# Kernel tuning notes

Measured on AMD Instinct MI355X. Metric: run time of the kernel, lower is better.

## Reference

```python
import jax, jax.numpy as jnp
import numpy as np

N_INST, L = 512, 512
VOCAB, EMB = 50000, 128
NF, K = 128, 3
HID = 3 * NF
ATT = 128
NCLS = 53


def setup_inputs() -> dict:
    key = jax.random.key(0)
    ks = jax.random.split(key, 10)
    char_ids = jax.random.randint(ks[0], (N_INST, L), 1, VOCAB)  # avoid pad_id=0
    pos_e1 = jax.random.randint(ks[1], (N_INST,), 0, L - 1)
    pos_e2 = jax.random.randint(ks[2], (N_INST,), 0, L - 1)
    emb = jax.random.normal(ks[3], (VOCAB, EMB), jnp.float32) * 0.02
    emb = emb.at[0].set(0.0)  # padding_idx = 0
    conv_w = jax.random.normal(ks[4], (NF, EMB, K), jnp.float32) * (1.0 / np.sqrt(EMB * K))
    conv_b = jnp.zeros((NF,), jnp.float32)
    W_w = jax.random.normal(ks[5], (ATT, HID), jnp.float32) * (1.0 / np.sqrt(HID))
    W_b = jnp.zeros((ATT,), jnp.float32)
    u_w = jax.random.normal(ks[6], (ATT,), jnp.float32) * (1.0 / np.sqrt(ATT))
    fc_w = jax.random.normal(ks[7], (NCLS, HID), jnp.float32) * (1.0 / np.sqrt(HID))
    fc_b = jnp.zeros((NCLS,), jnp.float32)
    return dict(char_ids=char_ids, pos_e1=pos_e1, pos_e2=pos_e2, emb=emb,
                conv_w=conv_w, conv_b=conv_b, W_w=W_w, W_b=W_b, u_w=u_w,
                fc_w=fc_w, fc_b=fc_b)


def _pcnn_pooled(char_ids, pos_e1, pos_e2, emb, conv_w, conv_b):
    # embedding lookup: (N, L, E) -> (N, E, L)
    x = jnp.transpose(emb[char_ids], (0, 2, 1))
    y = jax.lax.conv_general_dilated(
        x, conv_w, window_strides=(1,), padding=[(K // 2, K // 2)],
        dimension_numbers=('NCH', 'OIH', 'NCH'))
    y = jax.nn.relu(y + conv_b[None, :, None])  # (N, F, L)

    # per-row clamped/sorted boundaries (mirrors torch loop logic)
    e1 = jnp.minimum(pos_e1, pos_e2)
    e2 = jnp.maximum(pos_e1, pos_e2)
    e1 = jnp.clip(e1, 0, L)
    e2 = jnp.clip(e2, 0, L)
    e2 = jnp.where(e1 == e2, jnp.minimum(e1 + 1, L), e2)

    pos = jnp.arange(L)
    end1 = jnp.where(e1 > 0, e1, 1)                       # s1: [:e1] or [:1]
    m1 = pos[None, :] < end1[:, None]
    m2 = (pos[None, :] >= e1[:, None]) & (pos[None, :] < e2[:, None])  # s2: [e1:e2]
    m3 = jnp.where((e2 < L)[:, None], pos[None, :] >= e2[:, None],
                   pos[None, :] == L - 1)                 # s3: [e2:] or last col

    neg = jnp.finfo(y.dtype).min

    def mmax(m):
        return jnp.where(m[:, None, :], y, neg).max(axis=-1)  # (N, F)

    return jnp.concatenate([mmax(m1), mmax(m2), mmax(m3)], axis=-1)  # (N, 3F)


def reference(char_ids, pos_e1, pos_e2, emb, conv_w, conv_b, W_w, W_b, u_w, fc_w, fc_b):
    H = _pcnn_pooled(char_ids, pos_e1, pos_e2, emb, conv_w, conv_b)  # (N, HID)
    e = jnp.tanh(H @ W_w.T + W_b)            # (N, ATT)
    scores = e @ u_w                         # (N,)
    attn = jax.nn.softmax(scores, axis=0)    # (N,)
    h_bag = attn @ H                         # (HID,)
    logits = h_bag @ fc_w.T + fc_b           # (NCLS,)
    return logits, attn
```

## Files before the change

### kernel.cpp

```cpp
#include <hip/hip_runtime.h>
#include <hip/hip_bf16.h>
#include <math.h>
#include <float.h>

#define N_INST 512
#define LSEQ 512
#define EMB 128
#define NF 128
#define KW 3
#define HID 384
#define ATT 128
#define NCLS 53

#define XCOLS 66
#define XCOL_STRIDE 136

typedef __attribute__((ext_vector_type(8))) short short8;
typedef __attribute__((ext_vector_type(4))) float f32x4;

__global__ __launch_bounds__(256) void zero_kernel(float* __restrict__ H) {
  int i = blockIdx.x * 256 + threadIdx.x;
  if (i < N_INST * HID) H[i] = 0.0f;
}

__global__ __launch_bounds__(256) void prep_kernel(const float* __restrict__ conv_w,
                                                   const float* __restrict__ W_w,
                                                   ushort* __restrict__ whi,
                                                   ushort* __restrict__ wlo,
                                                   float* __restrict__ wwt) {
  int i = blockIdx.x * 256 + threadIdx.x;
  {
    int ii = i & 7;
    int L  = (i >> 3) & 63;
    int mf = (i >> 9) & 7;
    int eb = (i >> 12) & 3;
    int kk = (i >> 14);
    int f = mf * 16 + (L & 15);
    int e = eb * 32 + (L >> 4) * 8 + ii;
    float v = conv_w[(f * EMB + e) * KW + kk];
    __hip_bfloat16 hb = __float2bfloat16(v);
    float hf = __bfloat162float(hb);
    __hip_bfloat16 lb = __float2bfloat16(v - hf);
    whi[i] = *reinterpret_cast<ushort*>(&hb);
    wlo[i] = *reinterpret_cast<ushort*>(&lb);
  }
  {
    int a = i / HID;
    int h = i % HID;
    wwt[h * ATT + a] = W_w[i];
  }
}

__global__ __launch_bounds__(256) void pcnn_kernel(
    const int* __restrict__ char_ids, const int* __restrict__ pos_e1,
    const int* __restrict__ pos_e2, const float* __restrict__ emb,
    const float* __restrict__ conv_b, const ushort* __restrict__ whi,
    const ushort* __restrict__ wlo, float* __restrict__ H) {
  __shared__ ushort xh[XCOLS * XCOL_STRIDE];
  __shared__ ushort xl[XCOLS * XCOL_STRIDE];

  const int n = blockIdx.x >> 3;
  const int c0 = (blockIdx.x & 7) * 64;
  const int t = threadIdx.x;

  {
    const int q = t & 3;
    for (int j = (t >> 2); j < XCOLS; j += 64) {
      int g = c0 - 1 + j;
      ushort* dh = xh + j * XCOL_STRIDE + q * 32;
      ushort* dl = xl + j * XCOL_STRIDE + q * 32;
      if ((unsigned)g < (unsigned)LSEQ) {
        int cid = char_ids[n * LSEQ + g];
        const float* er = emb + cid * EMB + q * 32;
#pragma unroll
        for (int c = 0; c < 4; ++c) {
          float4 v0 = *(const float4*)(er + c * 8);
          float4 v1 = *(const float4*)(er + c * 8 + 4);
          float vv[8] = {v0.x, v0.y, v0.z, v0.w, v1.x, v1.y, v1.z, v1.w};
          short8 hvec, lvec;
#pragma unroll
          for (int w = 0; w < 8; ++w) {
            __hip_bfloat16 hb = __float2bfloat16(vv[w]);
            float hf = __bfloat162float(hb);
            __hip_bfloat16 lb = __float2bfloat16(vv[w] - hf);
            hvec[w] = (short)*reinterpret_cast<ushort*>(&hb);
            lvec[w] = (short)*reinterpret_cast<ushort*>(&lb);
          }
          *(short8*)(dh + c * 8) = hvec;
          *(short8*)(dl + c * 8) = lvec;
        }
      } else {
        short8 z = {0, 0, 0, 0, 0, 0, 0, 0};
#pragma unroll
        for (int c = 0; c < 4; ++c) {
          *(short8*)(dh + c * 8) = z;
          *(short8*)(dl + c * 8) = z;
        }
      }
    }
  }
  __syncthreads();

  const int wv = t >> 6;
  const int L = t & 63;
  const int lc = L & 15;
  const int lg = L >> 4;

  f32x4 acc[2][4];
  const f32x4 zz = {0.f, 0.f, 0.f, 0.f};
#pragma unroll
  for (int mf = 0; mf < 2; ++mf)
#pragma unroll
    for (int nf = 0; nf < 4; ++nf) acc[mf][nf] = zz;

  for (int eb = 0; eb < 4; ++eb) {
#pragma unroll
    for (int kk = 0; kk < 3; ++kk) {
      short8 ah[2], al[2];
#pragma unroll
      for (int mf = 0; mf < 2; ++mf) {
        int fragi = ((kk * 4 + eb) * 8 + (wv * 2 + mf)) * 64 + L;
        ah[mf] = *(const short8*)(whi + fragi * 8);
        al[mf] = *(const short8*)(wlo + fragi * 8);
      }
#pragma unroll
      for (int nf = 0; nf < 4; ++nf) {
        int off = (nf * 16 + kk + lc) * XCOL_STRIDE + eb * 32 + lg * 8;
        short8 bh = *(const short8*)(xh + off);
        short8 bl = *(const short8*)(xl + off);
#pragma unroll
        for (int mf = 0; mf < 2; ++mf) {
          acc[mf][nf] = __builtin_amdgcn_mfma_f32_16x16x32_bf16(ah[mf], bh, acc[mf][nf], 0, 0, 0);
          acc[mf][nf] = __builtin_amdgcn_mfma_f32_16x16x32_bf16(ah[mf], bl, acc[mf][nf], 0, 0, 0);
          acc[mf][nf] = __builtin_amdgcn_mfma_f32_16x16x32_bf16(al[mf], bh, acc[mf][nf], 0, 0, 0);
        }
      }
    }
  }

  int p1 = pos_e1[n], p2 = pos_e2[n];
  int e1v = min(p1, p2), e2v = max(p1, p2);
  e1v = min(max(e1v, 0), LSEQ);
  e2v = min(max(e2v, 0), LSEQ);
  if (e1v == e2v) e2v = min(e1v + 1, LSEQ);
  const int end1 = (e1v > 0) ? e1v : 1;

#pragma unroll
  for (int mf = 0; mf < 2; ++mf) {
#pragma unroll
    for (int r = 0; r < 4; ++r) {
      int f = wv * 32 + mf * 16 + lg * 4 + r;
      float bias = conv_b[f];
      float m1 = -FLT_MAX, m2 = -FLT_MAX, m3 = -FLT_MAX;
#pragma unroll
      for (int nf = 0; nf < 4; ++nf) {
        int l = c0 + nf * 16 + lc;
        float y = fmaxf(acc[mf][nf][r] + bias, 0.0f);
        if (l < end1) m1 = fmaxf(m1, y);
        if (l >= e1v && l < e2v) m2 = fmaxf(m2, y);
        bool in3 = (e2v < LSEQ) ? (l >= e2v) : (l == LSEQ - 1);
        if (in3) m3 = fmaxf(m3, y);
      }
#pragma unroll
      for (int off = 1; off < 16; off <<= 1) {
        m1 = fmaxf(m1, __shfl_xor(m1, off, 64));
        m2 = fmaxf(m2, __shfl_xor(m2, off, 64));
        m3 = fmaxf(m3, __shfl_xor(m3, off, 64));
      }
      if (lc == 0) {
        if (m1 >= 0.0f) atomicMax((int*)&H[n * HID + 0 * NF + f], __float_as_int(m1));
        if (m2 >= 0.0f) atomicMax((int*)&H[n * HID + 1 * NF + f], __float_as_int(m2));
        if (m3 >= 0.0f) atomicMax((int*)&H[n * HID + 2 * NF + f], __float_as_int(m3));
      }
    }
  }
}

__global__ __launch_bounds__(128) void score_kernel(
    const float* __restrict__ H, const float* __restrict__ wwt,
    const float* __restrict__ W_b, const float* __restrict__ u_w,
    float* __restrict__ scores) {
  __shared__ float Hrow[HID];
  __shared__ float red2[128];
  const int n = blockIdx.x;
  const int t = threadIdx.x;
#pragma unroll
  for (int s = 0; s < 3; ++s) Hrow[s * NF + t] = H[n * HID + s * NF + t];
  __syncthreads();
  float ss = W_b[t];
#pragma unroll 8
  for (int h = 0; h < HID; ++h) ss = fmaf(Hrow[h], wwt[h * ATT + t], ss);
  red2[t] = tanhf(ss) * u_w[t];
  __syncthreads();
  for (int off = 64; off > 0; off >>= 1) {
    if (t < off) red2[t] += red2[t + off];
    __syncthreads();
  }
  if (t == 0) scores[n] = red2[0];
}

__global__ __launch_bounds__(256) void finalize_kernel(
    const float* __restrict__ scores, const float* __restrict__ H,
    const float* __restrict__ fc_w, const float* __restrict__ fc_b,
    float* __restrict__ out) {
  __shared__ float sattn[N_INST];
  __shared__ float sred[256];
  __shared__ float hbag[HID];
  const int t = threadIdx.x;
  float s0 = scores[t];
  float s1 = scores[t + 256];
  sred[t] = fmaxf(s0, s1);
  __syncthreads();
  for (int off = 128; off > 0; off >>= 1) {
    if (t < off) sred[t] = fmaxf(sred[t], sred[t + off]);
    __syncthreads();
  }
  float mx = sred[0];
  __syncthreads();
  float ex0 = expf(s0 - mx), ex1 = expf(s1 - mx);
  sred[t] = ex0 + ex1;
  __syncthreads();
  for (int off = 128; off > 0; off >>= 1) {
    if (t < off) sred[t] += sred[t + off];
    __syncthreads();
  }
  float inv = 1.0f / sred[0];
  float a0 = ex0 * inv, a1 = ex1 * inv;
  sattn[t] = a0;
  sattn[t + 256] = a1;
  out[NCLS + t] = a0;
  out[NCLS + 256 + t] = a1;
  __syncthreads();

  for (int cc = t; cc < HID; cc += 256) {
    float acc = 0.0f;
    for (int n2 = 0; n2 < N_INST; ++n2) acc = fmaf(sattn[n2], H[n2 * HID + cc], acc);
    hbag[cc] = acc;
  }
  __syncthreads();
  if (t < NCLS) {
    float acc = fc_b[t];
    for (int h = 0; h < HID; ++h) acc = fmaf(hbag[h], fc_w[t * HID + h], acc);
    out[t] = acc;
  }
}

extern "C" void kernel_launch(void* const* d_in, const int* in_sizes, int n_in,
                              void* d_out, int out_size, void* d_ws, size_t ws_size,
                              hipStream_t stream) {
  const int* char_ids = (const int*)d_in[0];
  const int* pos_e1 = (const int*)d_in[1];
  const int* pos_e2 = (const int*)d_in[2];
  const float* emb = (const float*)d_in[3];
  const float* conv_w = (const float*)d_in[4];
  const float* conv_b = (const float*)d_in[5];
  const float* W_w = (const float*)d_in[6];
  const float* W_b = (const float*)d_in[7];
  const float* u_w = (const float*)d_in[8];
  const float* fc_w = (const float*)d_in[9];
  const float* fc_b = (const float*)d_in[10];
  float* out = (float*)d_out;

  ushort* whi = (ushort*)d_ws;
  ushort* wlo = whi + NF * EMB * KW;
  float* wwt = (float*)(wlo + NF * EMB * KW);
  float* H = wwt + ATT * HID;
  float* scores = H + N_INST * HID;

  hipLaunchKernelGGL(zero_kernel, dim3((N_INST * HID + 255) / 256), dim3(256), 0, stream, H);
  hipLaunchKernelGGL(prep_kernel, dim3(192), dim3(256), 0, stream, conv_w, W_w, whi, wlo, wwt);
  hipLaunchKernelGGL(pcnn_kernel, dim3(N_INST * 8), dim3(256), 0, stream,
                     char_ids, pos_e1, pos_e2, emb, conv_b, whi, wlo, H);
  hipLaunchKernelGGL(score_kernel, dim3(N_INST), dim3(128), 0, stream, H, wwt, W_b, u_w, scores);
  hipLaunchKernelGGL(finalize_kernel, dim3(1), dim3(256), 0, stream, scores, H, fc_w, fc_b, out);
}
```

Baseline: 241.4 us.

## Fuse conv, pooling and attention scoring into one block per instance

Each block now processes a whole instance: it loops over eight 64-column chunks, keeps the segment max-pool accumulators in registers, combines them through shared memory, and then computes the attention score in the same kernel. This removes the zero-fill kernel, the global atomicMax traffic on H and the separate score launch. In exchange, parallelism drops from 4096 blocks of 256 threads to 512 blocks of 512 threads, and each chunk adds serialized barriers between staging and compute with no overlap.

```diff
diff --git a/kernel.cpp b/kernel.cpp
--- a/kernel.cpp
+++ b/kernel.cpp
@@ -17,11 +17,6 @@
 
 typedef __attribute__((ext_vector_type(8))) short short8;
 typedef __attribute__((ext_vector_type(4))) float f32x4;
-
-__global__ __launch_bounds__(256) void zero_kernel(float* __restrict__ H) {
-  int i = blockIdx.x * 256 + threadIdx.x;
-  if (i < N_INST * HID) H[i] = 0.0f;
-}
 
 __global__ __launch_bounds__(256) void prep_kernel(const float* __restrict__ conv_w,
                                                    const float* __restrict__ W_w,
@@ -32,10 +27,10 @@
   {
     int ii = i & 7;
     int L  = (i >> 3) & 63;
-    int mf = (i >> 9) & 7;
+    int mf8 = (i >> 9) & 7;
     int eb = (i >> 12) & 3;
     int kk = (i >> 14);
-    int f = mf * 16 + (L & 15);
+    int f = mf8 * 16 + (L & 15);
     int e = eb * 32 + (L >> 4) * 8 + ii;
     float v = conv_w[(f * EMB + e) * KW + kk];
     __hip_bfloat16 hb = __float2bfloat16(v);
@@ -51,92 +46,27 @@
   }
 }
 
-__global__ __launch_bounds__(256) void pcnn_kernel(
+__global__ __launch_bounds__(512) void pcnn_kernel(
     const int* __restrict__ char_ids, const int* __restrict__ pos_e1,
     const int* __restrict__ pos_e2, const float* __restrict__ emb,
     const float* __restrict__ conv_b, const ushort* __restrict__ whi,
-    const ushort* __restrict__ wlo, float* __restrict__ H) {
+    const ushort* __restrict__ wlo, const float* __restrict__ wwt,
+    const float* __restrict__ W_b, const float* __restrict__ u_w,
+    float* __restrict__ H, float* __restrict__ scores) {
   __shared__ ushort xh[XCOLS * XCOL_STRIDE];
   __shared__ ushort xl[XCOLS * XCOL_STRIDE];
-
-  const int n = blockIdx.x >> 3;
-  const int c0 = (blockIdx.x & 7) * 64;
+  __shared__ float smAll[2][HID];
+  __shared__ float Hrow[HID];
+  __shared__ float red2[128];
+
+  const int n = blockIdx.x;
   const int t = threadIdx.x;
-
-  {
-    const int q = t & 3;
-    for (int j = (t >> 2); j < XCOLS; j += 64) {
-      int g = c0 - 1 + j;
-      ushort* dh = xh + j * XCOL_STRIDE + q * 32;
-      ushort* dl = xl + j * XCOL_STRIDE + q * 32;
-      if ((unsigned)g < (unsigned)LSEQ) {
-        int cid = char_ids[n * LSEQ + g];
-        const float* er = emb + cid * EMB + q * 32;
-#pragma unroll
-        for (int c = 0; c < 4; ++c) {
-          float4 v0 = *(const float4*)(er + c * 8);
-          float4 v1 = *(const float4*)(er + c * 8 + 4);
-          float vv[8] = {v0.x, v0.y, v0.z, v0.w, v1.x, v1.y, v1.z, v1.w};
-          short8 hvec, lvec;
-#pragma unroll
-          for (int w = 0; w < 8; ++w) {
-            __hip_bfloat16 hb = __float2bfloat16(vv[w]);
-            float hf = __bfloat162float(hb);
-            __hip_bfloat16 lb = __float2bfloat16(vv[w] - hf);
-            hvec[w] = (short)*reinterpret_cast<ushort*>(&hb);
-            lvec[w] = (short)*reinterpret_cast<ushort*>(&lb);
-          }
-          *(short8*)(dh + c * 8) = hvec;
-          *(short8*)(dl + c * 8) = lvec;
-        }
-      } else {
-        short8 z = {0, 0, 0, 0, 0, 0, 0, 0};
-#pragma unroll
-        for (int c = 0; c < 4; ++c) {
-          *(short8*)(dh + c * 8) = z;
-          *(short8*)(dl + c * 8) = z;
-        }
-      }
-    }
-  }
-  __syncthreads();
-
   const int wv = t >> 6;
+  const int fg = wv >> 1;
+  const int ch2 = wv & 1;
   const int L = t & 63;
   const int lc = L & 15;
   const int lg = L >> 4;
-
-  f32x4 acc[2][4];
-  const f32x4 zz = {0.f, 0.f, 0.f, 0.f};
-#pragma unroll
-  for (int mf = 0; mf < 2; ++mf)
-#pragma unroll
-    for (int nf = 0; nf < 4; ++nf) acc[mf][nf] = zz;
-
-  for (int eb = 0; eb < 4; ++eb) {
-#pragma unroll
-    for (int kk = 0; kk < 3; ++kk) {
-      short8 ah[2], al[2];
-#pragma unroll
-      for (int mf = 0; mf < 2; ++mf) {
-        int fragi = ((kk * 4 + eb) * 8 + (wv * 2 + mf)) * 64 + L;
-        ah[mf] = *(const short8*)(whi + fragi * 8);
-        al[mf] = *(const short8*)(wlo + fragi * 8);
-      }
-#pragma unroll
-      for (int nf = 0; nf < 4; ++nf) {
-        int off = (nf * 16 + kk + lc) * XCOL_STRIDE + eb * 32 + lg * 8;
-        short8 bh = *(const short8*)(xh + off);
-        short8 bl = *(const short8*)(xl + off);
-#pragma unroll
-        for (int mf = 0; mf < 2; ++mf) {
-          acc[mf][nf] = __builtin_amdgcn_mfma_f32_16x16x32_bf16(ah[mf], bh, acc[mf][nf], 0, 0, 0);
-          acc[mf][nf] = __builtin_amdgcn_mfma_f32_16x16x32_bf16(ah[mf], bl, acc[mf][nf], 0, 0, 0);
-          acc[mf][nf] = __builtin_amdgcn_mfma_f32_16x16x32_bf16(al[mf], bh, acc[mf][nf], 0, 0, 0);
-        }
-      }
-    }
-  }
 
   int p1 = pos_e1[n], p2 = pos_e2[n];
   int e1v = min(p1, p2), e2v = max(p1, p2);
@@ -145,22 +75,118 @@
   if (e1v == e2v) e2v = min(e1v + 1, LSEQ);
   const int end1 = (e1v > 0) ? e1v : 1;
 
-#pragma unroll
-  for (int mf = 0; mf < 2; ++mf) {
+  float biasv[2][4];
+#pragma unroll
+  for (int mf = 0; mf < 2; ++mf)
+#pragma unroll
+    for (int r = 0; r < 4; ++r)
+      biasv[mf][r] = conv_b[fg * 32 + mf * 16 + lg * 4 + r];
+
+  float sm1[2][4], sm2[2][4], sm3[2][4];
+#pragma unroll
+  for (int mf = 0; mf < 2; ++mf)
 #pragma unroll
     for (int r = 0; r < 4; ++r) {
-      int f = wv * 32 + mf * 16 + lg * 4 + r;
-      float bias = conv_b[f];
-      float m1 = -FLT_MAX, m2 = -FLT_MAX, m3 = -FLT_MAX;
-#pragma unroll
-      for (int nf = 0; nf < 4; ++nf) {
-        int l = c0 + nf * 16 + lc;
-        float y = fmaxf(acc[mf][nf][r] + bias, 0.0f);
-        if (l < end1) m1 = fmaxf(m1, y);
-        if (l >= e1v && l < e2v) m2 = fmaxf(m2, y);
-        bool in3 = (e2v < LSEQ) ? (l >= e2v) : (l == LSEQ - 1);
-        if (in3) m3 = fmaxf(m3, y);
-      }
+      sm1[mf][r] = -FLT_MAX; sm2[mf][r] = -FLT_MAX; sm3[mf][r] = -FLT_MAX;
+    }
+
+  const f32x4 zz = {0.f, 0.f, 0.f, 0.f};
+
+  for (int ch = 0; ch < 8; ++ch) {
+    const int c0 = ch * 64;
+    __syncthreads();
+
+    {
+      const int q8 = t & 7;
+      for (int j = (t >> 3); j < XCOLS; j += 64) {
+        int g = c0 - 1 + j;
+        ushort* dh = xh + j * XCOL_STRIDE + q8 * 16;
+        ushort* dl = xl + j * XCOL_STRIDE + q8 * 16;
+        if ((unsigned)g < (unsigned)LSEQ) {
+          int cid = char_ids[n * LSEQ + g];
+          const float* er = emb + cid * EMB + q8 * 16;
+#pragma unroll
+          for (int c = 0; c < 2; ++c) {
+            float4 v0 = *(const float4*)(er + c * 8);
+            float4 v1 = *(const float4*)(er + c * 8 + 4);
+            float vv[8] = {v0.x, v0.y, v0.z, v0.w, v1.x, v1.y, v1.z, v1.w};
+            short8 hvec, lvec;
+#pragma unroll
+            for (int w = 0; w < 8; ++w) {
+              __hip_bfloat16 hb = __float2bfloat16(vv[w]);
+              float hf = __bfloat162float(hb);
+              __hip_bfloat16 lb = __float2bfloat16(vv[w] - hf);
+              hvec[w] = (short)*reinterpret_cast<ushort*>(&hb);
+              lvec[w] = (short)*reinterpret_cast<ushort*>(&lb);
+            }
+            *(short8*)(dh + c * 8) = hvec;
+            *(short8*)(dl + c * 8) = lvec;
+          }
+        } else {
+          short8 z = {0, 0, 0, 0, 0, 0, 0, 0};
+#pragma unroll
+          for (int c = 0; c < 2; ++c) {
+            *(short8*)(dh + c * 8) = z;
+            *(short8*)(dl + c * 8) = z;
+          }
+        }
+      }
+    }
+    __syncthreads();
+
+    f32x4 acc[2][2];
+#pragma unroll
+    for (int mf = 0; mf < 2; ++mf)
+#pragma unroll
+      for (int nf = 0; nf < 2; ++nf) acc[mf][nf] = zz;
+
+    for (int eb = 0; eb < 4; ++eb) {
+#pragma unroll
+      for (int kk = 0; kk < 3; ++kk) {
+        short8 ah[2], al[2];
+#pragma unroll
+        for (int mf = 0; mf < 2; ++mf) {
+          int fragi = ((kk * 4 + eb) * 8 + (fg * 2 + mf)) * 64 + L;
+          ah[mf] = *(const short8*)(whi + fragi * 8);
+          al[mf] = *(const short8*)(wlo + fragi * 8);
+        }
+#pragma unroll
+        for (int nf = 0; nf < 2; ++nf) {
+          int off = (ch2 * 32 + nf * 16 + kk + lc) * XCOL_STRIDE + eb * 32 + lg * 8;
+          short8 bh = *(const short8*)(xh + off);
+          short8 bl = *(const short8*)(xl + off);
+#pragma unroll
+          for (int mf = 0; mf < 2; ++mf) {
+            acc[mf][nf] = __builtin_amdgcn_mfma_f32_16x16x32_bf16(ah[mf], bh, acc[mf][nf], 0, 0, 0);
+            acc[mf][nf] = __builtin_amdgcn_mfma_f32_16x16x32_bf16(ah[mf], bl, acc[mf][nf], 0, 0, 0);
+            acc[mf][nf] = __builtin_amdgcn_mfma_f32_16x16x32_bf16(al[mf], bh, acc[mf][nf], 0, 0, 0);
+          }
+        }
+      }
+    }
+
+#pragma unroll
+    for (int mf = 0; mf < 2; ++mf)
+#pragma unroll
+      for (int r = 0; r < 4; ++r) {
+        const float bias = biasv[mf][r];
+#pragma unroll
+        for (int nf = 0; nf < 2; ++nf) {
+          int l = c0 + ch2 * 32 + nf * 16 + lc;
+          float y = fmaxf(acc[mf][nf][r] + bias, 0.0f);
+          if (l < end1) sm1[mf][r] = fmaxf(sm1[mf][r], y);
+          if (l >= e1v && l < e2v) sm2[mf][r] = fmaxf(sm2[mf][r], y);
+          bool in3 = (e2v < LSEQ) ? (l >= e2v) : (l == LSEQ - 1);
+          if (in3) sm3[mf][r] = fmaxf(sm3[mf][r], y);
+        }
+      }
+  }
+
+#pragma unroll
+  for (int mf = 0; mf < 2; ++mf)
+#pragma unroll
+    for (int r = 0; r < 4; ++r) {
+      float m1 = sm1[mf][r], m2 = sm2[mf][r], m3 = sm3[mf][r];
 #pragma unroll
       for (int off = 1; off < 16; off <<= 1) {
         m1 = fmaxf(m1, __shfl_xor(m1, off, 64));
@@ -168,29 +194,26 @@
         m3 = fmaxf(m3, __shfl_xor(m3, off, 64));
       }
       if (lc == 0) {
-        if (m1 >= 0.0f) atomicMax((int*)&H[n * HID + 0 * NF + f], __float_as_int(m1));
-        if (m2 >= 0.0f) atomicMax((int*)&H[n * HID + 1 * NF + f], __float_as_int(m2));
-        if (m3 >= 0.0f) atomicMax((int*)&H[n * HID + 2 * NF + f], __float_as_int(m3));
-      }
-    }
-  }
-}
-
-__global__ __launch_bounds__(128) void score_kernel(
-    const float* __restrict__ H, const float* __restrict__ wwt,
-    const float* __restrict__ W_b, const float* __restrict__ u_w,
-    float* __restrict__ scores) {
-  __shared__ float Hrow[HID];
-  __shared__ float red2[128];
-  const int n = blockIdx.x;
-  const int t = threadIdx.x;
-#pragma unroll
-  for (int s = 0; s < 3; ++s) Hrow[s * NF + t] = H[n * HID + s * NF + t];
-  __syncthreads();
-  float ss = W_b[t];
+        int f = fg * 32 + mf * 16 + lg * 4 + r;
+        smAll[ch2][0 * NF + f] = m1;
+        smAll[ch2][1 * NF + f] = m2;
+        smAll[ch2][2 * NF + f] = m3;
+      }
+    }
+  __syncthreads();
+  if (t < HID) {
+    float v = fmaxf(smAll[0][t], smAll[1][t]);
+    Hrow[t] = v;
+    H[n * HID + t] = v;
+  }
+  __syncthreads();
+
+  if (t < ATT) {
+    float ss = W_b[t];
 #pragma unroll 8
-  for (int h = 0; h < HID; ++h) ss = fmaf(Hrow[h], wwt[h * ATT + t], ss);
-  red2[t] = tanhf(ss) * u_w[t];
+    for (int h = 0; h < HID; ++h) ss = fmaf(Hrow[h], wwt[h * ATT + t], ss);
+    red2[t] = tanhf(ss) * u_w[t];
+  }
   __syncthreads();
   for (int off = 64; off > 0; off >>= 1) {
     if (t < off) red2[t] += red2[t + off];
@@ -267,10 +290,8 @@
   float* H = wwt + ATT * HID;
   float* scores = H + N_INST * HID;
 
-  hipLaunchKernelGGL(zero_kernel, dim3((N_INST * HID + 255) / 256), dim3(256), 0, stream, H);
   hipLaunchKernelGGL(prep_kernel, dim3(192), dim3(256), 0, stream, conv_w, W_w, whi, wlo, wwt);
-  hipLaunchKernelGGL(pcnn_kernel, dim3(N_INST * 8), dim3(256), 0, stream,
-                     char_ids, pos_e1, pos_e2, emb, conv_b, whi, wlo, H);
-  hipLaunchKernelGGL(score_kernel, dim3(N_INST), dim3(128), 0, stream, H, wwt, W_b, u_w, scores);
+  hipLaunchKernelGGL(pcnn_kernel, dim3(N_INST), dim3(512), 0, stream,
+                     char_ids, pos_e1, pos_e2, emb, conv_b, whi, wlo, wwt, W_b, u_w, H, scores);
   hipLaunchKernelGGL(finalize_kernel, dim3(1), dim3(256), 0, stream, scores, H, fc_w, fc_b, out);
 }
```

New measurement: 263.0 us. 9.0% more time.
